# Kernel optimization log

Hardware: AMD Instinct MI355X
Metric: run time of the kernel (lower is better)

The kernel has to match this reference:

```python
import jax, jax.numpy as jnp
import numpy as np

N = 100000   # nodes
E = 1000000  # edges
G = 64       # graphs in batch
DIN, DH, DOUT = 128, 128, 64
BN_EPS = 1e-5


def setup_inputs() -> dict:
    key = jax.random.key(0)
    ks = jax.random.split(key, 20)
    inp = {}
    inp['x'] = jax.random.normal(ks[0], (N, DIN), dtype=jnp.float32)
    inp['edge_index'] = jax.random.randint(ks[1], (2, E), 0, N, dtype=jnp.int64)
    inp['batch'] = jnp.sort(jax.random.randint(ks[2], (N,), 0, G, dtype=jnp.int64))
    # GCN conv weights (stored [in, out]) + biases
    s = lambda k, i, o: jax.random.normal(k, (i, o), dtype=jnp.float32) / np.sqrt(i)
    inp['W1'] = s(ks[3], DIN, DH);  inp['b1'] = jnp.zeros((DH,), jnp.float32)
    inp['W2'] = s(ks[4], DH, DH);   inp['b2'] = jnp.zeros((DH,), jnp.float32)
    inp['W3'] = s(ks[5], DH, DOUT); inp['b3'] = jnp.zeros((DOUT,), jnp.float32)
    # BatchNorm params/buffers (eval mode)
    inp['g1'] = jnp.ones((DH,), jnp.float32);  inp['beta1'] = jnp.zeros((DH,), jnp.float32)
    inp['g2'] = jnp.ones((DH,), jnp.float32);  inp['beta2'] = jnp.zeros((DH,), jnp.float32)
    inp['mean1'] = jnp.zeros((DH,), jnp.float32); inp['var1'] = jnp.ones((DH,), jnp.float32)
    inp['mean2'] = jnp.zeros((DH,), jnp.float32); inp['var2'] = jnp.ones((DH,), jnp.float32)
    # GlobalAttention gate_nn: Linear(DOUT,DH) ReLU Linear(DH,1)
    inp['Wg1'] = s(ks[6], DOUT, DH); inp['bg1'] = jnp.zeros((DH,), jnp.float32)
    inp['Wg2'] = s(ks[7], DH, 1);    inp['bg2'] = jnp.zeros((1,), jnp.float32)
    # head MLP: Linear(DOUT,DH) ReLU Linear(DH,DOUT)
    inp['Wm1'] = s(ks[8], DOUT, DH); inp['bm1'] = jnp.zeros((DH,), jnp.float32)
    inp['Wm2'] = s(ks[9], DH, DOUT); inp['bm2'] = jnp.zeros((DOUT,), jnp.float32)
    return inp


def _gcn_conv(x, W, b, src, dst):
    # PyG GCNConv: add self-loops, sym-normalize, linear, scatter-sum, bias
    h = x @ W                                            # [N, out]
    deg = jnp.ones((N,), h.dtype).at[dst].add(1.0)       # in-degree + self-loop
    dinv = jax.lax.rsqrt(deg)
    norm = dinv[src] * dinv[dst]                         # [E]
    msg = h[src] * norm[:, None]                         # gather + scale
    out = jax.ops.segment_sum(msg, dst, num_segments=N)  # scatter
    out = out + h * (dinv * dinv)[:, None]               # self-loop term
    return out + b


def _bn(x, g, beta, mean, var):
    return (x - mean) * jax.lax.rsqrt(var + BN_EPS) * g + beta


def reference(x, edge_index, batch, W1, b1, W2, b2, W3, b3,
              g1, beta1, g2, beta2, mean1, var1, mean2, var2,
              Wg1, bg1, Wg2, bg2, Wm1, bm1, Wm2, bm2):
    src, dst = edge_index[0], edge_index[1]
    h = jax.nn.relu(_bn(_gcn_conv(x, W1, b1, src, dst), g1, beta1, mean1, var1))
    h = jax.nn.relu(_bn(_gcn_conv(h, W2, b2, src, dst), g2, beta2, mean2, var2))
    h = _gcn_conv(h, W3, b3, src, dst)                   # [N, DOUT]
    # GlobalAttention pooling: per-graph softmax of gate scores
    gate = jax.nn.relu(h @ Wg1 + bg1) @ Wg2 + bg2        # [N, 1]
    gate = gate[:, 0]
    m = jax.ops.segment_max(gate, batch, num_segments=G)
    e = jnp.exp(gate - m[batch])
    s = jax.ops.segment_sum(e, batch, num_segments=G)
    a = e / s[batch]                                     # [N]
    pooled = jax.ops.segment_sum(h * a[:, None], batch, num_segments=G)  # [G, DOUT]
    # MLP head (dropout off in eval)
    return jax.nn.relu(pooled @ Wm1 + bm1) @ Wm2 + bm2   # [G, DOUT]
```

## Files before the change

### kernel.cpp

```cpp
#include <hip/hip_runtime.h>
#include <hip/hip_bf16.h>
#include <hip/hip_fp16.h>
#include <math.h>

#define NN 100000
#define EE 1000000
#define GG 64
#define BN_EPS 1e-5f
#define CPB 16
#define EB 4096
#define NBLK ((EE + EB - 1) / EB)
#define NBUCK ((NN + 511) / 512)

typedef __attribute__((ext_vector_type(8))) short bf16x8;
typedef __attribute__((ext_vector_type(4))) float f32x4;

__device__ inline short f2bf(float f) {
  unsigned u = __float_as_uint(f);
  u = u + 0x7fff + ((u >> 16) & 1);
  return (short)(u >> 16);
}
__device__ inline float bf2f(short h) {
  return __uint_as_float(((unsigned)(unsigned short)h) << 16);
}

__device__ inline unsigned fenc(float f) {
  int b = __float_as_int(f);
  return (b < 0) ? ~(unsigned)b : ((unsigned)b | 0x80000000u);
}
__device__ inline float fdec(unsigned u) {
  int b = (u & 0x80000000u) ? (int)(u & 0x7fffffffu) : (int)~u;
  return __int_as_float(b);
}

__device__ inline void acc2(float& a0, float& a1, unsigned u) {
  asm("v_fma_mix_f32 %0, %2, 1.0, %0 op_sel:[0,0,0] op_sel_hi:[1,0,0]\n\t"
      "v_fma_mix_f32 %1, %2, 1.0, %1 op_sel:[1,0,0] op_sel_hi:[1,0,0]"
      : "+v"(a0), "+v"(a1)
      : "v"(u));
}
__device__ inline void acc8(float* a, uint4 u) {
  acc2(a[0], a[1], u.x);
  acc2(a[2], a[3], u.y);
  acc2(a[4], a[5], u.z);
  acc2(a[6], a[7], u.w);
}
__device__ inline uint4 zsel(uint4 u, int ok) {
  uint4 r;
  r.x = ok ? u.x : 0u;
  r.y = ok ? u.y : 0u;
  r.z = ok ? u.z : 0u;
  r.w = ok ? u.w : 0u;
  return r;
}

__global__ __launch_bounds__(256) void k_bhist(const int* __restrict__ dst,
                                               int* __restrict__ bhist, int E) {
  __shared__ int h[256];
  int t = threadIdx.x;
  h[t] = 0;
  __syncthreads();
  int base = blockIdx.x * EB;
#pragma unroll
  for (int j = 0; j < EB / 256; ++j) {
    int i = base + j * 256 + t;
    if (i < E) atomicAdd(&h[dst[i] >> 9], 1);
  }
  __syncthreads();
  bhist[blockIdx.x * 256 + t] = h[t];
}

__global__ __launch_bounds__(256) void k_bscan1(int* __restrict__ bhist,
                                                int* __restrict__ btot) {
  __shared__ int s[256];
  int bin = blockIdx.x, t = threadIdx.x;
  int v = (t < NBLK) ? bhist[t * 256 + bin] : 0;
  s[t] = v;
  __syncthreads();
  for (int o = 1; o < 256; o <<= 1) {
    int u = (t >= o) ? s[t - o] : 0;
    __syncthreads();
    s[t] += u;
    __syncthreads();
  }
  if (t < NBLK) bhist[t * 256 + bin] = s[t] - v;
  if (t == 255) btot[bin] = s[255];
}

__global__ __launch_bounds__(256) void k_bscan2(const int* __restrict__ btot,
                                                int* __restrict__ bstart) {
  __shared__ int s[256];
  int t = threadIdx.x;
  int v = btot[t];
  s[t] = v;
  __syncthreads();
  for (int o = 1; o < 256; o <<= 1) {
    int u = (t >= o) ? s[t - o] : 0;
    __syncthreads();
    s[t] += u;
    __syncthreads();
  }
  bstart[t] = s[t] - v;
}

__global__ __launch_bounds__(256) void k_bscat(const int* __restrict__ src,
                                               const int* __restrict__ dst,
                                               const int* __restrict__ bhist,
                                               const int* __restrict__ bstart,
                                               int2* __restrict__ pairs, int E) {
  __shared__ int h[256];
  __shared__ int base[256];
  int t = threadIdx.x;
  h[t] = 0;
  __syncthreads();
  int b0 = blockIdx.x * EB;
  int ds[EB / 256], rk[EB / 256];
#pragma unroll
  for (int j = 0; j < EB / 256; ++j) {
    int i = b0 + j * 256 + t;
    if (i < E) {
      int d = dst[i];
      ds[j] = d;
      rk[j] = atomicAdd(&h[d >> 9], 1);
    } else
      ds[j] = -1;
  }
  __syncthreads();
  base[t] = bstart[t] + bhist[blockIdx.x * 256 + t];
  __syncthreads();
#pragma unroll
  for (int j = 0; j < EB / 256; ++j) {
    int i = b0 + j * 256 + t;
    if (ds[j] >= 0) {
      int pos = base[ds[j] >> 9] + rk[j];
      pairs[pos] = make_int2(src[i], ds[j]);
    }
  }
}

__global__ __launch_bounds__(256) void k_bfill(const int2* __restrict__ pairs,
                                               const int* __restrict__ bstart,
                                               int* __restrict__ rowstart,
                                               int* __restrict__ eidx,
                                               float* __restrict__ dinv, int N,
                                               int E) {
  __shared__ int h[512];
  __shared__ int ex[512];
  __shared__ int ps[256];
  const int b = blockIdx.x;
  const int n0 = b << 9;
  const int e0 = bstart[b], e1 = bstart[b + 1];
  const int t = threadIdx.x;
  h[t] = 0;
  h[t + 256] = 0;
  __syncthreads();
  for (int i = e0 + t; i < e1; i += 256) atomicAdd(&h[pairs[i].y - n0], 1);
  __syncthreads();
  int v0 = h[2 * t], v1 = h[2 * t + 1];
  int sp = v0 + v1;
  ps[t] = sp;
  __syncthreads();
  for (int o = 1; o < 256; o <<= 1) {
    int u = (t >= o) ? ps[t - o] : 0;
    __syncthreads();
    ps[t] += u;
    __syncthreads();
  }
  int ex0 = ps[t] - sp;
  ex[2 * t] = ex0;
  ex[2 * t + 1] = ex0 + v0;
  __syncthreads();
  for (int i = t; i < 512; i += 256) {
    int node = n0 + i;
    if (node < N) {
      rowstart[node] = e0 + ex[i];
      dinv[node] = rsqrtf(1.0f + (float)h[i]);
    }
  }
  if (b == 0 && t == 0) rowstart[N] = E;
  __syncthreads();
  for (int i = e0 + t; i < e1; i += 256) {
    int2 p = pairs[i];
    int r = atomicAdd(&ex[p.y - n0], 1);
    eidx[e0 + r] = p.x;
  }
}

__global__ __launch_bounds__(256) void k_prep(
    const float* __restrict__ W1, const float* __restrict__ W2,
    const float* __restrict__ W3, const float* __restrict__ Wg1,
    short* __restrict__ wt, const float* __restrict__ g1,
    const float* __restrict__ b1, const float* __restrict__ m1,
    const float* __restrict__ v1, const float* __restrict__ g2,
    const float* __restrict__ b2, const float* __restrict__ m2,
    const float* __restrict__ v2, float* __restrict__ s1,
    float* __restrict__ h1, float* __restrict__ s2, float* __restrict__ h2,
    const int* __restrict__ batch, int* __restrict__ gstart,
    float* __restrict__ pooledw, int N) {
  const int b = blockIdx.x, t = threadIdx.x;
  if (b < 192) {
    int i = b * 256 + t;
    const float* W;
    short *hi, *lo;
    int K, M, idx;
    if (i < 16384) {
      W = W1; hi = wt; lo = wt + 16384; K = 128; M = 128; idx = i;
    } else if (i < 32768) {
      W = W2; hi = wt + 32768; lo = wt + 49152; K = 128; M = 128; idx = i - 16384;
    } else if (i < 40960) {
      W = W3; hi = wt + 65536; lo = wt + 73728; K = 128; M = 64; idx = i - 32768;
    } else {
      W = Wg1; hi = wt + 81920; lo = wt + 90112; K = 64; M = 128; idx = i - 40960;
    }
    int k = idx / M, n = idx % M;
    float w = W[idx];
    short h = f2bf(w);
    hi[n * K + k] = h;
    lo[n * K + k] = f2bf(w - bf2f(h));
  } else if (b == 192) {
    if (t < 128) {
      float s = g1[t] * rsqrtf(v1[t] + BN_EPS);
      s1[t] = s;
      h1[t] = b1[t] - m1[t] * s;
    } else {
      int j = t - 128;
      float s = g2[j] * rsqrtf(v2[j] + BN_EPS);
      s2[j] = s;
      h2[j] = b2[j] - m2[j] * s;
    }
  } else {
    if (t <= GG) {
      int lo = 0, hi = N;
      while (lo < hi) {
        int mid = (lo + hi) >> 1;
        if (batch[mid] < t) lo = mid + 1;
        else hi = mid;
      }
      gstart[t] = lo;
    }
    for (int i = t; i < GG * 64 + GG + GG; i += 256) pooledw[i] = 0.f;
  }
}

template <int K, int M, int CTB, int AIN, int DINV, int OUTH>
__device__ __forceinline__ void mgemm_body(
    short* lds, const float* __restrict__ Xf, const short* __restrict__ Xhi,
    const short* __restrict__ Xlo, const short* __restrict__ Wthi,
    const short* __restrict__ Wtlo, const float* __restrict__ dinv,
    void* __restrict__ Y, int nrows) {
  constexpr int NC = K / 32;
  constexpr int KP = K + 8;
  constexpr int R = 2;
  const int lane = threadIdx.x & 63;
  const int wave = threadIdx.x >> 6;
  const int m16 = lane & 15;
  const int quad = lane >> 4;
  const int rowbase = blockIdx.x * 128 + wave * 32;
  const int cbase = blockIdx.y * CTB * 16;

  bf16x8 ahi[R][NC], alo[R][NC];
#pragma unroll
  for (int t = 0; t < R; ++t) {
    const int arow = rowbase + t * 16 + m16;
    const bool rok = arow < nrows;
#pragma unroll
    for (int c = 0; c < NC; ++c) {
      const int k0 = c * 32 + quad * 8;
      if constexpr (AIN) {
        if (rok) {
          ahi[t][c] = *(const bf16x8*)(Xhi + (size_t)arow * K + k0);
          alo[t][c] = *(const bf16x8*)(Xlo + (size_t)arow * K + k0);
        } else {
          ahi[t][c] = bf16x8{0, 0, 0, 0, 0, 0, 0, 0};
          alo[t][c] = bf16x8{0, 0, 0, 0, 0, 0, 0, 0};
        }
      } else {
        float4 v0 = make_float4(0.f, 0.f, 0.f, 0.f), v1 = v0;
        if (rok) {
          v0 = *(const float4*)(Xf + (size_t)arow * K + k0);
          v1 = *(const float4*)(Xf + (size_t)arow * K + k0 + 4);
        }
        float vv[8] = {v0.x, v0.y, v0.z, v0.w, v1.x, v1.y, v1.z, v1.w};
#pragma unroll
        for (int j = 0; j < 8; ++j) {
          short h = f2bf(vv[j]);
          ahi[t][c][j] = h;
          alo[t][c][j] = f2bf(vv[j] - bf2f(h));
        }
      }
    }
  }

  {
    constexpr int ELEMS = CTB * 16 * K;
#pragma unroll
    for (int i = threadIdx.x * 8; i < ELEMS; i += 256 * 8) {
      const int r = i / K, c = i % K;
      *(bf16x8*)(&lds[r * KP + c]) =
          *(const bf16x8*)(Wthi + (size_t)(cbase + r) * K + c);
      *(bf16x8*)(&lds[CTB * 16 * KP + r * KP + c]) =
          *(const bf16x8*)(Wtlo + (size_t)(cbase + r) * K + c);
    }
  }

  float dv[R][4];
  if constexpr (DINV) {
#pragma unroll
    for (int t = 0; t < R; ++t)
#pragma unroll
      for (int r = 0; r < 4; ++r) {
        int row = rowbase + t * 16 + quad * 4 + r;
        dv[t][r] = (row < nrows) ? dinv[row] : 0.f;
      }
  }

  __syncthreads();

  f32x4 accs[CTB][R];
#pragma unroll
  for (int ct = 0; ct < CTB; ++ct) {
    bf16x8 bhi[NC], blo[NC];
    const int wrow = (ct * 16 + m16) * KP + quad * 8;
#pragma unroll
    for (int c = 0; c < NC; ++c) {
      bhi[c] = *(const bf16x8*)(&lds[wrow + c * 32]);
      blo[c] = *(const bf16x8*)(&lds[CTB * 16 * KP + wrow + c * 32]);
    }
#pragma unroll
    for (int t = 0; t < R; ++t) {
      f32x4 acc = {0.f, 0.f, 0.f, 0.f};
#pragma unroll
      for (int c = 0; c < NC; ++c) {
        acc = __builtin_amdgcn_mfma_f32_16x16x32_bf16(ahi[t][c], bhi[c], acc, 0, 0, 0);
        acc = __builtin_amdgcn_mfma_f32_16x16x32_bf16(ahi[t][c], blo[c], acc, 0, 0, 0);
        acc = __builtin_amdgcn_mfma_f32_16x16x32_bf16(alo[t][c], bhi[c], acc, 0, 0, 0);
      }
      accs[ct][t] = acc;
    }
  }

  constexpr int COLS = CTB * 16;
  constexpr int SP = COLS + 8;
  __syncthreads();
#pragma unroll
  for (int ct = 0; ct < CTB; ++ct)
#pragma unroll
    for (int t = 0; t < R; ++t)
#pragma unroll
      for (int r = 0; r < 4; ++r) {
        const int row_l = wave * 32 + t * 16 + quad * 4 + r;
        float v = accs[ct][t][r];
        if constexpr (DINV) v *= dv[t][r];
        __half hv = __float2half(v);
        lds[row_l * SP + ct * 16 + m16] = *(short*)&hv;
      }
  __syncthreads();
  constexpr int TOT = 128 * COLS;
#pragma unroll
  for (int p = 0; p < TOT / (256 * 8); ++p) {
    const int idx8 = (p * 256 + threadIdx.x) * 8;
    const int row_l = idx8 / COLS;
    const int col0 = idx8 % COLS;
    const int grow = blockIdx.x * 128 + row_l;
    if (grow < nrows) {
      bf16x8 v = *(const bf16x8*)(&lds[row_l * SP + col0]);
      *(bf16x8*)((__half*)Y + (size_t)grow * M + cbase + col0) = v;
    }
  }
}

#define MGEMM_ARGS                                                            \
  const float *Xf, const short *Xhi, const short *Xlo, const short *Wthi,     \
      const short *Wtlo, const float *dinv, void *Y, int nrows

#define DEF_MGEMM(NAME, K, M, CTB, AIN, DINV, OUTH)                           \
  __global__ __launch_bounds__(256, 3) void NAME(MGEMM_ARGS) {                \
    __shared__ short lds[2 * CTB * 16 * (K + 8)];                             \
    mgemm_body<K, M, CTB, AIN, DINV, OUTH>(lds, Xf, Xhi, Xlo, Wthi, Wtlo,     \
                                           dinv, Y, nrows);                   \
  }

DEF_MGEMM(k_mgemm1, 128, 128, 4, 0, 1, 1)
DEF_MGEMM(k_mgemm2, 128, 128, 4, 1, 1, 1)
DEF_MGEMM(k_mgemm3, 128, 64, 4, 1, 1, 1)

template <int M, int EPI>
__device__ __forceinline__ void agg_body(
    const __half* __restrict__ hp, const int* __restrict__ rowstart,
    const int* __restrict__ eidx, const float* __restrict__ dinv,
    const float* __restrict__ bias, const float* __restrict__ bns,
    const float* __restrict__ bnh, float* __restrict__ outf,
    short* __restrict__ ohi, short* __restrict__ olo, int N) {
  constexpr int LPR = M / 8;
  constexpr int NPW = 64 / (2 * LPR);
  const int wv = (blockIdx.x * 256 + threadIdx.x) >> 6;
  const int lane = threadIdx.x & 63;
  const int grp = lane / (2 * LPR);
  const int slot = (lane / LPR) & 1;
  const int sub = lane % LPR;
  const int w = wv * NPW + grp;
  if (w >= N) return;
  const unsigned subo = (unsigned)sub * 16u;
  const float di = dinv[w];
  const int lo = rowstart[w], hi = rowstart[w + 1];
  const int hi1 = hi - 1;
  const char* hpb = (const char*)hp;
  float a[8] = {0.f, 0.f, 0.f, 0.f, 0.f, 0.f, 0.f, 0.f};

  int e = lo + slot;
  while (e < hi) {
    int idx[8], ss[8];
    uint4 uu[8];
#pragma unroll
    for (int p = 0; p < 8; ++p) {
      idx[p] = e + 2 * p;
      ss[p] = eidx[min(idx[p], hi1)];
    }
#pragma unroll
    for (int p = 0; p < 8; ++p)
      uu[p] = *(const uint4*)(hpb + ((unsigned)ss[p] * (unsigned)(M * 2) + subo));
#pragma unroll
    for (int p = 0; p < 8; ++p) {
      uu[p] = zsel(uu[p], idx[p] < hi);
      acc8(a, uu[p]);
    }
    e += 16;
  }
#pragma unroll
  for (int j = 0; j < 8; ++j) a[j] += __shfl_xor(a[j], LPR, 64);

  if (slot != 0) return;
  uint4 us = *(const uint4*)(hpb + ((unsigned)w * (unsigned)(M * 2) + subo));
  acc8(a, us);
  float4 b0 = *(const float4*)(bias + sub * 8);
  float4 b1 = *(const float4*)(bias + sub * 8 + 4);
  float r[8];
  r[0] = a[0] * di + b0.x;
  r[1] = a[1] * di + b0.y;
  r[2] = a[2] * di + b0.z;
  r[3] = a[3] * di + b0.w;
  r[4] = a[4] * di + b1.x;
  r[5] = a[5] * di + b1.y;
  r[6] = a[6] * di + b1.z;
  r[7] = a[7] * di + b1.w;
  if constexpr (EPI) {
    float4 s0 = *(const float4*)(bns + sub * 8);
    float4 s1 = *(const float4*)(bns + sub * 8 + 4);
    float4 h0 = *(const float4*)(bnh + sub * 8);
    float4 h1 = *(const float4*)(bnh + sub * 8 + 4);
    float sv[8] = {s0.x, s0.y, s0.z, s0.w, s1.x, s1.y, s1.z, s1.w};
    float hv[8] = {h0.x, h0.y, h0.z, h0.w, h1.x, h1.y, h1.z, h1.w};
    short hs[8], ls[8];
#pragma unroll
    for (int j = 0; j < 8; ++j) {
      float ev = fmaxf(r[j] * sv[j] + hv[j], 0.f);
      short hb = f2bf(ev);
      float res = ev - bf2f(hb);
      hs[j] = hb;
      ls[j] = (short)(__float_as_uint(res) >> 16);
    }
    *(short4*)(ohi + (size_t)w * M + sub * 8) = make_short4(hs[0], hs[1], hs[2], hs[3]);
    *(short4*)(ohi + (size_t)w * M + sub * 8 + 4) = make_short4(hs[4], hs[5], hs[6], hs[7]);
    *(short4*)(olo + (size_t)w * M + sub * 8) = make_short4(ls[0], ls[1], ls[2], ls[3]);
    *(short4*)(olo + (size_t)w * M + sub * 8 + 4) = make_short4(ls[4], ls[5], ls[6], ls[7]);
  } else {
    *(float4*)(outf + (size_t)w * M + sub * 8) = make_float4(r[0], r[1], r[2], r[3]);
    *(float4*)(outf + (size_t)w * M + sub * 8 + 4) = make_float4(r[4], r[5], r[6], r[7]);
  }
}

#define AGG_ARGS                                                              \
  const __half *hp, const int *rowstart, const int *eidx, const float *dinv,  \
      const float *bias, const float *bns, const float *bnh, float *outf,     \
      short *ohi, short *olo, int N

#define DEF_AGG(NAME, M, EPI)                                                 \
  __global__ __launch_bounds__(256) void NAME(AGG_ARGS) {                     \
    agg_body<M, EPI>(hp, rowstart, eidx, dinv, bias, bns, bnh, outf, ohi,     \
                     olo, N);                                                 \
  }

DEF_AGG(k_agg1, 128, 1)
DEF_AGG(k_agg2, 128, 1)

__global__ __launch_bounds__(256) void k_agg3g(
    const __half* __restrict__ hp, const int* __restrict__ rowstart,
    const int* __restrict__ eidx, const float* __restrict__ dinv,
    const float* __restrict__ bias, const short* __restrict__ wg1hi,
    const short* __restrict__ wg1lo, const float* __restrict__ bg1,
    const float* __restrict__ Wg2v, const float* __restrict__ bg2v,
    float* __restrict__ outf, float* __restrict__ gate, int N) {
  __shared__ short Ahi[16][72];
  __shared__ short Alo[16][72];
  const int lane = threadIdx.x & 63;
  const int wv = threadIdx.x >> 6;
  const int grp = lane >> 4;
  const int slot = (lane >> 3) & 1;
  const int sub = lane & 7;
  const int node_l = wv * 4 + grp;
  const int w = blockIdx.x * 16 + node_l;
  const bool valid = w < N;

  for (int i = threadIdx.x; i < 16 * 72; i += 256) {
    (&Ahi[0][0])[i] = 0;
    (&Alo[0][0])[i] = 0;
  }
  __syncthreads();

  const unsigned subo = (unsigned)sub * 16u;
  const float di = valid ? dinv[w] : 0.f;
  const int lo = valid ? rowstart[w] : 0;
  const int hi = valid ? rowstart[w + 1] : 0;
  const int hi1 = hi - 1;
  const char* hpb = (const char*)hp;
  float a[8] = {0.f, 0.f, 0.f, 0.f, 0.f, 0.f, 0.f, 0.f};

  int e = lo + slot;
  while (e < hi) {
    int idx[8], ss[8];
    uint4 uu[8];
#pragma unroll
    for (int p = 0; p < 8; ++p) {
      idx[p] = e + 2 * p;
      ss[p] = eidx[min(idx[p], hi1)];
    }
#pragma unroll
    for (int p = 0; p < 8; ++p)
      uu[p] = *(const uint4*)(hpb + ((unsigned)ss[p] * 128u + subo));
#pragma unroll
    for (int p = 0; p < 8; ++p) {
      uu[p] = zsel(uu[p], idx[p] < hi);
      acc8(a, uu[p]);
    }
    e += 16;
  }
#pragma unroll
  for (int j = 0; j < 8; ++j) a[j] += __shfl_xor(a[j], 8, 64);

  if (slot == 0 && valid) {
    uint4 us = *(const uint4*)(hpb + ((unsigned)w * 128u + subo));
    acc8(a, us);
    float4 b0 = *(const float4*)(bias + sub * 8);
    float4 b1 = *(const float4*)(bias + sub * 8 + 4);
    float r[8];
    r[0] = a[0] * di + b0.x;
    r[1] = a[1] * di + b0.y;
    r[2] = a[2] * di + b0.z;
    r[3] = a[3] * di + b0.w;
    r[4] = a[4] * di + b1.x;
    r[5] = a[5] * di + b1.y;
    r[6] = a[6] * di + b1.z;
    r[7] = a[7] * di + b1.w;
    *(float4*)(outf + (size_t)w * 64 + sub * 8) =
        make_float4(r[0], r[1], r[2], r[3]);
    *(float4*)(outf + (size_t)w * 64 + sub * 8 + 4) =
        make_float4(r[4], r[5], r[6], r[7]);
#pragma unroll
    for (int j = 0; j < 8; ++j) {
      short h = f2bf(r[j]);
      Ahi[node_l][sub * 8 + j] = h;
      Alo[node_l][sub * 8 + j] = f2bf(r[j] - bf2f(h));
    }
  }
  __syncthreads();

  if (wv != 0) return;
  const int m16 = lane & 15;
  const int quad = lane >> 4;
  bf16x8 fa_hi[2], fa_lo[2];
#pragma unroll
  for (int c = 0; c < 2; ++c) {
    fa_hi[c] = *(const bf16x8*)(&Ahi[m16][c * 32 + quad * 8]);
    fa_lo[c] = *(const bf16x8*)(&Alo[m16][c * 32 + quad * 8]);
  }
  float gp[4] = {0.f, 0.f, 0.f, 0.f};
#pragma unroll
  for (int ct = 0; ct < 8; ++ct) {
    bf16x8 bhi[2], blo[2];
    const int wrow = (ct * 16 + m16) * 64 + quad * 8;
#pragma unroll
    for (int c = 0; c < 2; ++c) {
      bhi[c] = *(const bf16x8*)(wg1hi + wrow + c * 32);
      blo[c] = *(const bf16x8*)(wg1lo + wrow + c * 32);
    }
    f32x4 acc = {0.f, 0.f, 0.f, 0.f};
#pragma unroll
    for (int c = 0; c < 2; ++c) {
      acc = __builtin_amdgcn_mfma_f32_16x16x32_bf16(fa_hi[c], bhi[c], acc, 0, 0, 0);
      acc = __builtin_amdgcn_mfma_f32_16x16x32_bf16(fa_hi[c], blo[c], acc, 0, 0, 0);
      acc = __builtin_amdgcn_mfma_f32_16x16x32_bf16(fa_lo[c], bhi[c], acc, 0, 0, 0);
    }
    const int col = ct * 16 + m16;
    const float gb = bg1[col], wg = Wg2v[col];
#pragma unroll
    for (int r = 0; r < 4; ++r) gp[r] += fmaxf(acc[r] + gb, 0.f) * wg;
  }
#pragma unroll
  for (int o = 1; o < 16; o <<= 1)
#pragma unroll
    for (int r = 0; r < 4; ++r) gp[r] += __shfl_xor(gp[r], o, 64);
  if (m16 == 0) {
    const float b2 = bg2v[0];
#pragma unroll
    for (int r = 0; r < 4; ++r) {
      const int node = blockIdx.x * 16 + quad * 4 + r;
      if (node < N) gate[node] = gp[r] + b2;
    }
  }
}

__global__ __launch_bounds__(256) void k_pmax(const float* __restrict__ gate,
                                              const int* __restrict__ gstart,
                                              unsigned* __restrict__ gmaxu) {
  __shared__ unsigned red[256];
  const int g = blockIdx.x / CPB;
  const int c = blockIdx.x % CPB;
  const int lo = gstart[g], hi = gstart[g + 1];
  const int len = hi - lo;
  const int b0 = lo + (int)(((long long)len * c) / CPB);
  const int b1 = lo + (int)(((long long)len * (c + 1)) / CPB);
  unsigned mx = 0u;
  for (int i = b0 + threadIdx.x; i < b1; i += 256) mx = max(mx, fenc(gate[i]));
  red[threadIdx.x] = mx;
  __syncthreads();
  for (int o = 128; o; o >>= 1) {
    if (threadIdx.x < o)
      red[threadIdx.x] = max(red[threadIdx.x], red[threadIdx.x + o]);
    __syncthreads();
  }
  if (threadIdx.x == 0 && red[0] != 0u) atomicMax(&gmaxu[g], red[0]);
}

__global__ __launch_bounds__(256) void k_psum(const float* __restrict__ gate,
                                              const float* __restrict__ h3,
                                              const unsigned* __restrict__ gmaxu,
                                              const int* __restrict__ gstart,
                                              float* __restrict__ pooledw,
                                              float* __restrict__ ssum) {
  __shared__ float accs[4][64];
  __shared__ float ses[4];
  const int g = blockIdx.x / CPB;
  const int c = blockIdx.x % CPB;
  const int lo = gstart[g], hi = gstart[g + 1];
  const int len = hi - lo;
  const int b0 = lo + (int)(((long long)len * c) / CPB);
  const int b1 = lo + (int)(((long long)len * (c + 1)) / CPB);
  const int wave = threadIdx.x >> 6, lane = threadIdx.x & 63;
  const float m = fdec(gmaxu[g]);
  float acc = 0.f, se = 0.f;
  for (int i = b0 + wave; i < b1; i += 4) {
    float e = expf(gate[i] - m);
    acc += e * h3[(size_t)i * 64 + lane];
    se += e;
  }
  accs[wave][lane] = acc;
  if (lane == 0) ses[wave] = se;
  __syncthreads();
  if (threadIdx.x < 64) {
    float a = accs[0][threadIdx.x] + accs[1][threadIdx.x] +
              accs[2][threadIdx.x] + accs[3][threadIdx.x];
    if (a != 0.f) atomicAdd(&pooledw[g * 64 + threadIdx.x], a);
  }
  if (threadIdx.x == 64) {
    float s = ses[0] + ses[1] + ses[2] + ses[3];
    if (s != 0.f) atomicAdd(&ssum[g], s);
  }
}

__global__ __launch_bounds__(256) void k_head(const float* __restrict__ pooledw,
                                              const float* __restrict__ ssum,
                                              const float* __restrict__ Wm1,
                                              const float* __restrict__ bm1,
                                              const float* __restrict__ Wm2,
                                              const float* __restrict__ bm2,
                                              float* __restrict__ out) {
  __shared__ float P[64 * 64];
  __shared__ float T[64 * 128];
  int tid = threadIdx.x;
  for (int i = tid; i < 4096; i += 256) {
    float s = ssum[i >> 6];
    P[i] = pooledw[i] * ((s > 0.f) ? 1.0f / s : 0.f);
  }
  __syncthreads();
  for (int e = tid; e < 8192; e += 256) {
    int r = e >> 7, c = e & 127;
    float a = bm1[c];
    for (int k = 0; k < 64; ++k) a += P[r * 64 + k] * Wm1[k * 128 + c];
    T[e] = fmaxf(a, 0.f);
  }
  __syncthreads();
  for (int e = tid; e < 4096; e += 256) {
    int r = e >> 6, c = e & 63;
    float a = bm2[c];
    for (int k = 0; k < 128; ++k) a += T[r * 128 + k] * Wm2[k * 64 + c];
    out[e] = a;
  }
}

extern "C" void kernel_launch(void* const* d_in, const int* in_sizes, int n_in,
                              void* d_out, int out_size, void* d_ws,
                              size_t ws_size, hipStream_t stream) {
  const int N = NN, E = EE;
  const float* x = (const float*)d_in[0];
  const int* ei = (const int*)d_in[1];
  const int* batch = (const int*)d_in[2];
  const float* W1 = (const float*)d_in[3];
  const float* b1 = (const float*)d_in[4];
  const float* W2 = (const float*)d_in[5];
  const float* b2 = (const float*)d_in[6];
  const float* W3 = (const float*)d_in[7];
  const float* b3 = (const float*)d_in[8];
  const float* g1 = (const float*)d_in[9];
  const float* beta1 = (const float*)d_in[10];
  const float* g2 = (const float*)d_in[11];
  const float* beta2 = (const float*)d_in[12];
  const float* mean1 = (const float*)d_in[13];
  const float* var1 = (const float*)d_in[14];
  const float* mean2 = (const float*)d_in[15];
  const float* var2 = (const float*)d_in[16];
  const float* Wg1 = (const float*)d_in[17];
  const float* bg1 = (const float*)d_in[18];
  const float* Wg2 = (const float*)d_in[19];
  const float* bg2 = (const float*)d_in[20];
  const float* Wm1 = (const float*)d_in[21];
  const float* bm1 = (const float*)d_in[22];
  const float* Wm2 = (const float*)d_in[23];
  const float* bm2 = (const float*)d_in[24];
  float* out = (float*)d_out;

  const int* src = ei;
  const int* dst = ei + E;

  char* wsb = (char*)d_ws;
  size_t off = 0;
  auto alloc = [&](size_t elems) -> void* {
    void* p = wsb + off;
    off += elems * 4;
    return p;
  };
  int* rowstart = (int*)alloc(N + 4);
  int* eidx = (int*)alloc(E);
  int2* pairs = (int2*)alloc((size_t)E * 2);
  int* bhist = (int*)alloc(NBLK * 256 + 256);
  int* btot = (int*)alloc(256);
  int* bstart = (int*)alloc(256);
  float* dinv = (float*)alloc(N);
  float* gate = (float*)alloc(N);
  __half* hbuf = (__half*)alloc((size_t)N * 64);
  short* ahi_p = (short*)alloc((size_t)N * 64);
  short* alo_p = (short*)alloc((size_t)N * 64);
  float* fbuf = (float*)alloc((size_t)N * 64);
  short* wt = (short*)alloc(49152);
  float* bn1s = (float*)alloc(128);
  float* bn1h = (float*)alloc(128);
  float* bn2s = (float*)alloc(128);
  float* bn2h = (float*)alloc(128);
  float* pooledw = (float*)alloc(GG * 64);
  float* ssum = (float*)alloc(GG);
  unsigned* gmaxu = (unsigned*)alloc(GG);
  int* gstart = (int*)alloc(GG + 4);
  (void)ws_size;
  (void)n_in;
  (void)in_sizes;
  (void)out_size;

  k_bhist<<<NBLK, 256, 0, stream>>>(dst, bhist, E);
  k_bscan1<<<256, 256, 0, stream>>>(bhist, btot);
  k_bscan2<<<1, 256, 0, stream>>>(btot, bstart);
  k_bscat<<<NBLK, 256, 0, stream>>>(src, dst, bhist, bstart, pairs, E);
  k_bfill<<<NBUCK, 256, 0, stream>>>(pairs, bstart, rowstart, eidx, dinv, N, E);

  k_prep<<<194, 256, 0, stream>>>(W1, W2, W3, Wg1, wt, g1, beta1, mean1, var1,
                                  g2, beta2, mean2, var2, bn1s, bn1h, bn2s,
                                  bn2h, batch, gstart, pooledw, N);

  const int gbb = (N + 127) / 128;
  const int ab128 = (N + 7) / 8;
  const int ab16 = (N + 15) / 16;

  k_mgemm1<<<dim3(gbb, 2), 256, 0, stream>>>(x, nullptr, nullptr, wt,
                                             wt + 16384, dinv, hbuf, N);
  k_agg1<<<ab128, 256, 0, stream>>>(hbuf, rowstart, eidx, dinv, b1, bn1s,
                                    bn1h, nullptr, ahi_p, alo_p, N);

  k_mgemm2<<<dim3(gbb, 2), 256, 0, stream>>>(nullptr, ahi_p, alo_p, wt + 32768,
                                             wt + 49152, dinv, hbuf, N);
  k_agg2<<<ab128, 256, 0, stream>>>(hbuf, rowstart, eidx, dinv, b2, bn2s,
                                    bn2h, nullptr, ahi_p, alo_p, N);

  k_mgemm3<<<dim3(gbb, 1), 256, 0, stream>>>(nullptr, ahi_p, alo_p, wt + 65536,
                                             wt + 73728, dinv, hbuf, N);
  k_agg3g<<<ab16, 256, 0, stream>>>(hbuf, rowstart, eidx, dinv, b3,
                                    wt + 81920, wt + 90112, bg1, Wg2, bg2,
                                    fbuf, gate, N);

  k_pmax<<<GG * CPB, 256, 0, stream>>>(gate, gstart, gmaxu);
  k_psum<<<GG * CPB, 256, 0, stream>>>(gate, fbuf, gmaxu, gstart, pooledw,
                                       ssum);

  k_head<<<1, 256, 0, stream>>>(pooledw, ssum, Wm1, bm1, Wm2, bm2, out);
}
```

Baseline: 455.6 us.

## Fuse aggregation epilogue with next layer's GEMM in one kernel

After: 457.0 us. No clear change (+0.3%).

```diff
diff --git a/kernel.cpp b/kernel.cpp
--- a/kernel.cpp
+++ b/kernel.cpp
@@ -242,15 +242,15 @@
   }
 }
 
-template <int K, int M, int CTB, int AIN, int DINV, int OUTH>
-__device__ __forceinline__ void mgemm_body(
-    short* lds, const float* __restrict__ Xf, const short* __restrict__ Xhi,
-    const short* __restrict__ Xlo, const short* __restrict__ Wthi,
+template <int K, int M, int CTB>
+__global__ __launch_bounds__(256, 3) void k_mgemm1(
+    const float* __restrict__ Xf, const short* __restrict__ Wthi,
     const short* __restrict__ Wtlo, const float* __restrict__ dinv,
-    void* __restrict__ Y, int nrows) {
+    __half* __restrict__ Y, int nrows) {
   constexpr int NC = K / 32;
   constexpr int KP = K + 8;
   constexpr int R = 2;
+  __shared__ short lds[2 * CTB * 16 * KP];
   const int lane = threadIdx.x & 63;
   const int wave = threadIdx.x >> 6;
   const int m16 = lane & 15;
@@ -266,27 +266,17 @@
 #pragma unroll
     for (int c = 0; c < NC; ++c) {
       const int k0 = c * 32 + quad * 8;
-      if constexpr (AIN) {
-        if (rok) {
-          ahi[t][c] = *(const bf16x8*)(Xhi + (size_t)arow * K + k0);
-          alo[t][c] = *(const bf16x8*)(Xlo + (size_t)arow * K + k0);
-        } else {
-          ahi[t][c] = bf16x8{0, 0, 0, 0, 0, 0, 0, 0};
-          alo[t][c] = bf16x8{0, 0, 0, 0, 0, 0, 0, 0};
-        }
-      } else {
-        float4 v0 = make_float4(0.f, 0.f, 0.f, 0.f), v1 = v0;
-        if (rok) {
-          v0 = *(const float4*)(Xf + (size_t)arow * K + k0);
-          v1 = *(const float4*)(Xf + (size_t)arow * K + k0 + 4);
-        }
-        float vv[8] = {v0.x, v0.y, v0.z, v0.w, v1.x, v1.y, v1.z, v1.w};
-#pragma unroll
-        for (int j = 0; j < 8; ++j) {
-          short h = f2bf(vv[j]);
-          ahi[t][c][j] = h;
-          alo[t][c][j] = f2bf(vv[j] - bf2f(h));
-        }
+      float4 v0 = make_float4(0.f, 0.f, 0.f, 0.f), v1 = v0;
+      if (rok) {
+        v0 = *(const float4*)(Xf + (size_t)arow * K + k0);
+        v1 = *(const float4*)(Xf + (size_t)arow * K + k0 + 4);
+      }
+      float vv[8] = {v0.x, v0.y, v0.z, v0.w, v1.x, v1.y, v1.z, v1.w};
+#pragma unroll
+      for (int j = 0; j < 8; ++j) {
+        short h = f2bf(vv[j]);
+        ahi[t][c][j] = h;
+        alo[t][c][j] = f2bf(vv[j] - bf2f(h));
       }
     }
   }
@@ -304,15 +294,13 @@
   }
 
   float dv[R][4];
-  if constexpr (DINV) {
-#pragma unroll
-    for (int t = 0; t < R; ++t)
-#pragma unroll
-      for (int r = 0; r < 4; ++r) {
-        int row = rowbase + t * 16 + quad * 4 + r;
-        dv[t][r] = (row < nrows) ? dinv[row] : 0.f;
-      }
-  }
+#pragma unroll
+  for (int t = 0; t < R; ++t)
+#pragma unroll
+    for (int r = 0; r < 4; ++r) {
+      int row = rowbase + t * 16 + quad * 4 + r;
+      dv[t][r] = (row < nrows) ? dinv[row] : 0.f;
+    }
 
   __syncthreads();
 
@@ -349,8 +337,7 @@
 #pragma unroll
       for (int r = 0; r < 4; ++r) {
         const int row_l = wave * 32 + t * 16 + quad * 4 + r;
-        float v = accs[ct][t][r];
-        if constexpr (DINV) v *= dv[t][r];
+        float v = accs[ct][t][r] * dv[t][r];
         __half hv = __float2half(v);
         lds[row_l * SP + ct * 16 + m16] = *(short*)&hv;
       }
@@ -364,45 +351,32 @@
     const int grow = blockIdx.x * 128 + row_l;
     if (grow < nrows) {
       bf16x8 v = *(const bf16x8*)(&lds[row_l * SP + col0]);
-      *(bf16x8*)((__half*)Y + (size_t)grow * M + cbase + col0) = v;
-    }
-  }
-}
-
-#define MGEMM_ARGS                                                            \
-  const float *Xf, const short *Xhi, const short *Xlo, const short *Wthi,     \
-      const short *Wtlo, const float *dinv, void *Y, int nrows
-
-#define DEF_MGEMM(NAME, K, M, CTB, AIN, DINV, OUTH)                           \
-  __global__ __launch_bounds__(256, 3) void NAME(MGEMM_ARGS) {                \
-    __shared__ short lds[2 * CTB * 16 * (K + 8)];                             \
-    mgemm_body<K, M, CTB, AIN, DINV, OUTH>(lds, Xf, Xhi, Xlo, Wthi, Wtlo,     \
-                                           dinv, Y, nrows);                   \
-  }
-
-DEF_MGEMM(k_mgemm1, 128, 128, 4, 0, 1, 1)
-DEF_MGEMM(k_mgemm2, 128, 128, 4, 1, 1, 1)
-DEF_MGEMM(k_mgemm3, 128, 64, 4, 1, 1, 1)
-
-template <int M, int EPI>
-__device__ __forceinline__ void agg_body(
+      *(bf16x8*)(Y + (size_t)grow * M + cbase + col0) = v;
+    }
+  }
+}
+
+template <int MOUT>
+__global__ __launch_bounds__(512) void k_aggf(
     const __half* __restrict__ hp, const int* __restrict__ rowstart,
     const int* __restrict__ eidx, const float* __restrict__ dinv,
     const float* __restrict__ bias, const float* __restrict__ bns,
-    const float* __restrict__ bnh, float* __restrict__ outf,
-    short* __restrict__ ohi, short* __restrict__ olo, int N) {
-  constexpr int LPR = M / 8;
-  constexpr int NPW = 64 / (2 * LPR);
-  const int wv = (blockIdx.x * 256 + threadIdx.x) >> 6;
+    const float* __restrict__ bnh, const short* __restrict__ wthi,
+    const short* __restrict__ wtlo, __half* __restrict__ hbout, int N) {
+  __shared__ short Ahi[16][136];
+  __shared__ short Alo[16][136];
+  __shared__ short St[16][MOUT + 8];
   const int lane = threadIdx.x & 63;
-  const int grp = lane / (2 * LPR);
-  const int slot = (lane / LPR) & 1;
-  const int sub = lane % LPR;
-  const int w = wv * NPW + grp;
-  if (w >= N) return;
+  const int wv = threadIdx.x >> 6;
+  const int node_l = wv * 2 + (lane >> 5);
+  const int slot = (lane >> 4) & 1;
+  const int sub = lane & 15;
+  const int w = blockIdx.x * 16 + node_l;
+  const bool valid = w < N;
   const unsigned subo = (unsigned)sub * 16u;
-  const float di = dinv[w];
-  const int lo = rowstart[w], hi = rowstart[w + 1];
+  const float di = valid ? dinv[w] : 0.f;
+  const int lo = valid ? rowstart[w] : 0;
+  const int hi = valid ? rowstart[w + 1] : 0;
   const int hi1 = hi - 1;
   const char* hpb = (const char*)hp;
   float a[8] = {0.f, 0.f, 0.f, 0.f, 0.f, 0.f, 0.f, 0.f};
@@ -418,7 +392,7 @@
     }
 #pragma unroll
     for (int p = 0; p < 8; ++p)
-      uu[p] = *(const uint4*)(hpb + ((unsigned)ss[p] * (unsigned)(M * 2) + subo));
+      uu[p] = *(const uint4*)(hpb + ((unsigned)ss[p] * 256u + subo));
 #pragma unroll
     for (int p = 0; p < 8; ++p) {
       uu[p] = zsel(uu[p], idx[p] < hi);
@@ -427,61 +401,97 @@
     e += 16;
   }
 #pragma unroll
-  for (int j = 0; j < 8; ++j) a[j] += __shfl_xor(a[j], LPR, 64);
-
-  if (slot != 0) return;
-  uint4 us = *(const uint4*)(hpb + ((unsigned)w * (unsigned)(M * 2) + subo));
-  acc8(a, us);
-  float4 b0 = *(const float4*)(bias + sub * 8);
-  float4 b1 = *(const float4*)(bias + sub * 8 + 4);
-  float r[8];
-  r[0] = a[0] * di + b0.x;
-  r[1] = a[1] * di + b0.y;
-  r[2] = a[2] * di + b0.z;
-  r[3] = a[3] * di + b0.w;
-  r[4] = a[4] * di + b1.x;
-  r[5] = a[5] * di + b1.y;
-  r[6] = a[6] * di + b1.z;
-  r[7] = a[7] * di + b1.w;
-  if constexpr (EPI) {
-    float4 s0 = *(const float4*)(bns + sub * 8);
-    float4 s1 = *(const float4*)(bns + sub * 8 + 4);
-    float4 h0 = *(const float4*)(bnh + sub * 8);
-    float4 h1 = *(const float4*)(bnh + sub * 8 + 4);
-    float sv[8] = {s0.x, s0.y, s0.z, s0.w, s1.x, s1.y, s1.z, s1.w};
-    float hv[8] = {h0.x, h0.y, h0.z, h0.w, h1.x, h1.y, h1.z, h1.w};
+  for (int j = 0; j < 8; ++j) a[j] += __shfl_xor(a[j], 16, 64);
+
+  if (slot == 0) {
     short hs[8], ls[8];
+    if (valid) {
+      uint4 us = *(const uint4*)(hpb + ((unsigned)w * 256u + subo));
+      acc8(a, us);
+      float4 b0 = *(const float4*)(bias + sub * 8);
+      float4 b1 = *(const float4*)(bias + sub * 8 + 4);
+      float r[8];
+      r[0] = a[0] * di + b0.x;
+      r[1] = a[1] * di + b0.y;
+      r[2] = a[2] * di + b0.z;
+      r[3] = a[3] * di + b0.w;
+      r[4] = a[4] * di + b1.x;
+      r[5] = a[5] * di + b1.y;
+      r[6] = a[6] * di + b1.z;
+      r[7] = a[7] * di + b1.w;
+      float4 s0 = *(const float4*)(bns + sub * 8);
+      float4 s1 = *(const float4*)(bns + sub * 8 + 4);
+      float4 h0 = *(const float4*)(bnh + sub * 8);
+      float4 h1 = *(const float4*)(bnh + sub * 8 + 4);
+      float sv[8] = {s0.x, s0.y, s0.z, s0.w, s1.x, s1.y, s1.z, s1.w};
+      float hv[8] = {h0.x, h0.y, h0.z, h0.w, h1.x, h1.y, h1.z, h1.w};
+#pragma unroll
+      for (int j = 0; j < 8; ++j) {
+        float ev = fmaxf(r[j] * sv[j] + hv[j], 0.f);
+        short hb = f2bf(ev);
+        float res = ev - bf2f(hb);
+        hs[j] = hb;
+        ls[j] = (short)(__float_as_uint(res) >> 16);
+      }
+    } else {
+#pragma unroll
+      for (int j = 0; j < 8; ++j) {
+        hs[j] = 0;
+        ls[j] = 0;
+      }
+    }
 #pragma unroll
     for (int j = 0; j < 8; ++j) {
-      float ev = fmaxf(r[j] * sv[j] + hv[j], 0.f);
-      short hb = f2bf(ev);
-      float res = ev - bf2f(hb);
-      hs[j] = hb;
-      ls[j] = (short)(__float_as_uint(res) >> 16);
-    }
-    *(short4*)(ohi + (size_t)w * M + sub * 8) = make_short4(hs[0], hs[1], hs[2], hs[3]);
-    *(short4*)(ohi + (size_t)w * M + sub * 8 + 4) = make_short4(hs[4], hs[5], hs[6], hs[7]);
-    *(short4*)(olo + (size_t)w * M + sub * 8) = make_short4(ls[0], ls[1], ls[2], ls[3]);
-    *(short4*)(olo + (size_t)w * M + sub * 8 + 4) = make_short4(ls[4], ls[5], ls[6], ls[7]);
-  } else {
-    *(float4*)(outf + (size_t)w * M + sub * 8) = make_float4(r[0], r[1], r[2], r[3]);
-    *(float4*)(outf + (size_t)w * M + sub * 8 + 4) = make_float4(r[4], r[5], r[6], r[7]);
-  }
-}
-
-#define AGG_ARGS                                                              \
-  const __half *hp, const int *rowstart, const int *eidx, const float *dinv,  \
-      const float *bias, const float *bns, const float *bnh, float *outf,     \
-      short *ohi, short *olo, int N
-
-#define DEF_AGG(NAME, M, EPI)                                                 \
-  __global__ __launch_bounds__(256) void NAME(AGG_ARGS) {                     \
-    agg_body<M, EPI>(hp, rowstart, eidx, dinv, bias, bns, bnh, outf, ohi,     \
-                     olo, N);                                                 \
-  }
-
-DEF_AGG(k_agg1, 128, 1)
-DEF_AGG(k_agg2, 128, 1)
+      Ahi[node_l][sub * 8 + j] = hs[j];
+      Alo[node_l][sub * 8 + j] = ls[j];
+    }
+  }
+  __syncthreads();
+
+  const int m16 = lane & 15;
+  const int quad = lane >> 4;
+  constexpr int CT = MOUT / 16;
+  if (wv < CT) {
+    bf16x8 fah[4], fal[4];
+#pragma unroll
+    for (int c = 0; c < 4; ++c) {
+      fah[c] = *(const bf16x8*)(&Ahi[m16][c * 32 + quad * 8]);
+      fal[c] = *(const bf16x8*)(&Alo[m16][c * 32 + quad * 8]);
+    }
+    bf16x8 bhi[4], blo[4];
+    const int wrow = (wv * 16 + m16) * 128 + quad * 8;
+#pragma unroll
+    for (int c = 0; c < 4; ++c) {
+      bhi[c] = *(const bf16x8*)(wthi + wrow + c * 32);
+      blo[c] = *(const bf16x8*)(wtlo + wrow + c * 32);
+    }
+    f32x4 acc = {0.f, 0.f, 0.f, 0.f};
+#pragma unroll
+    for (int c = 0; c < 4; ++c) {
+      acc = __builtin_amdgcn_mfma_f32_16x16x32_bf16(fah[c], bhi[c], acc, 0, 0, 0);
+      acc = __builtin_amdgcn_mfma_f32_16x16x32_bf16(fah[c], blo[c], acc, 0, 0, 0);
+      acc = __builtin_amdgcn_mfma_f32_16x16x32_bf16(fal[c], bhi[c], acc, 0, 0, 0);
+    }
+#pragma unroll
+    for (int r = 0; r < 4; ++r) {
+      const int grow = blockIdx.x * 16 + quad * 4 + r;
+      const float dvv = (grow < N) ? dinv[grow] : 0.f;
+      __half hv = __float2half(acc[r] * dvv);
+      St[quad * 4 + r][wv * 16 + m16] = *(short*)&hv;
+    }
+  }
+  __syncthreads();
+
+  constexpr int SEGS = MOUT / 8;
+  const int tid = threadIdx.x;
+  if (tid < 16 * SEGS) {
+    const int row = tid / SEGS, seg = tid % SEGS;
+    const int grow = blockIdx.x * 16 + row;
+    if (grow < N)
+      *(bf16x8*)(hbout + (size_t)grow * MOUT + seg * 8) =
+          *(const bf16x8*)(&St[row][seg * 8]);
+  }
+}
 
 __global__ __launch_bounds__(256) void k_agg3g(
     const __half* __restrict__ hp, const int* __restrict__ rowstart,
@@ -746,9 +756,8 @@
   int* bstart = (int*)alloc(256);
   float* dinv = (float*)alloc(N);
   float* gate = (float*)alloc(N);
-  __half* hbuf = (__half*)alloc((size_t)N * 64);
-  short* ahi_p = (short*)alloc((size_t)N * 64);
-  short* alo_p = (short*)alloc((size_t)N * 64);
+  __half* hbufA = (__half*)alloc((size_t)N * 64);
+  __half* hbufB = (__half*)alloc((size_t)N * 64);
   float* fbuf = (float*)alloc((size_t)N * 64);
   short* wt = (short*)alloc(49152);
   float* bn1s = (float*)alloc(128);
@@ -775,22 +784,16 @@
                                   bn2h, batch, gstart, pooledw, N);
 
   const int gbb = (N + 127) / 128;
-  const int ab128 = (N + 7) / 8;
   const int ab16 = (N + 15) / 16;
 
-  k_mgemm1<<<dim3(gbb, 2), 256, 0, stream>>>(x, nullptr, nullptr, wt,
-                                             wt + 16384, dinv, hbuf, N);
-  k_agg1<<<ab128, 256, 0, stream>>>(hbuf, rowstart, eidx, dinv, b1, bn1s,
-                                    bn1h, nullptr, ahi_p, alo_p, N);
-
-  k_mgemm2<<<dim3(gbb, 2), 256, 0, stream>>>(nullptr, ahi_p, alo_p, wt + 32768,
-                                             wt + 49152, dinv, hbuf, N);
-  k_agg2<<<ab128, 256, 0, stream>>>(hbuf, rowstart, eidx, dinv, b2, bn2s,
-                                    bn2h, nullptr, ahi_p, alo_p, N);
-
-  k_mgemm3<<<dim3(gbb, 1), 256, 0, stream>>>(nullptr, ahi_p, alo_p, wt + 65536,
-                                             wt + 73728, dinv, hbuf, N);
-  k_agg3g<<<ab16, 256, 0, stream>>>(hbuf, rowstart, eidx, dinv, b3,
+  k_mgemm1<128, 128, 4><<<dim3(gbb, 2), 256, 0, stream>>>(x, wt, wt + 16384,
+                                                          dinv, hbufA, N);
+  k_aggf<128><<<ab16, 512, 0, stream>>>(hbufA, rowstart, eidx, dinv, b1, bn1s,
+                                        bn1h, wt + 32768, wt + 49152, hbufB,
+                                        N);
+  k_aggf<64><<<ab16, 512, 0, stream>>>(hbufB, rowstart, eidx, dinv, b2, bn2s,
+                                       bn2h, wt + 65536, wt + 73728, hbufA, N);
+  k_agg3g<<<ab16, 256, 0, stream>>>(hbufA, rowstart, eidx, dinv, b3,
                                     wt + 81920, wt + 90112, bg1, Wg2, bg2,
                                     fbuf, gate, N);
 
```
